# Performance work log

Measured on AMD Instinct MI355X. Metric: run time of the kernel, lower is better.

Reference implementation:

```python
import jax, jax.numpy as jnp
import numpy as np

D_MODEL = 256
B, S = 4, 4096


def setup_inputs() -> dict:
    key = jax.random.key(0)
    ks = jax.random.split(key, 6)
    k = jax.random.normal(ks[0], (B, S, D_MODEL), dtype=jnp.float32)
    q = jax.random.normal(ks[1], (B, S, D_MODEL), dtype=jnp.float32)
    v = jax.random.normal(ks[2], (B, S, D_MODEL), dtype=jnp.float32)
    # causal mask: (S, S), 1 where attending is allowed, 0 elsewhere
    mask = jnp.tril(jnp.ones((S, S), dtype=jnp.int32))
    # nn.Linear(d, d, bias=False) weights, applied as x @ W.T
    scale = 1.0 / np.sqrt(D_MODEL)
    Wk = jax.random.uniform(ks[3], (D_MODEL, D_MODEL), jnp.float32, -scale, scale)
    Wq = jax.random.uniform(ks[4], (D_MODEL, D_MODEL), jnp.float32, -scale, scale)
    Wv = jax.random.uniform(ks[5], (D_MODEL, D_MODEL), jnp.float32, -scale, scale)
    return {"k": k, "q": q, "v": v, "Wk": Wk, "Wq": Wq, "Wv": Wv, "mask": mask}


def reference(k, q, v, Wk, Wq, Wv, mask):
    # projections: nn.Linear applies x @ W.T
    key = jnp.einsum('bsd,ed->bse', k, Wk)
    query = jnp.einsum('bsd,ed->bse', q, Wq)
    value = jnp.einsum('bsd,ed->bse', v, Wv)
    # scores (b, s_q, s_k), scaled by sqrt(d_model)
    logits = jnp.einsum('bqd,bkd->bqk', query, key) / jnp.sqrt(jnp.float32(query.shape[-1]))
    logits = jnp.where(mask[None, :, :] == 0, -jnp.inf, logits)
    probs = jax.nn.softmax(logits, axis=-1)
    # dropout p=0.0 (eval) -> identity
    return jnp.einsum('bqk,bkd->bqd', probs, value)
```

## Files before the change

kernel.cpp:

```cpp
#include <hip/hip_runtime.h>


typedef __bf16 bf16_t;
typedef bf16_t bf16x8 __attribute__((ext_vector_type(8)));
typedef bf16_t bf16x4 __attribute__((ext_vector_type(4)));
typedef float  f32x4  __attribute__((ext_vector_type(4)));
typedef float  f32x16 __attribute__((ext_vector_type(16)));
typedef unsigned int u32;
typedef u32 u32x4 __attribute__((ext_vector_type(4)));

#define MFMA16(a, b, c) __builtin_amdgcn_mfma_f32_16x16x32_bf16((a), (b), (c), 0, 0, 0)
#define MFMA32(a, b, c) __builtin_amdgcn_mfma_f32_32x32x16_bf16((a), (b), (c), 0, 0, 0)

#define GLOAD_LDS16(gsrc, ldst) \
    __builtin_amdgcn_global_load_lds( \
        (const __attribute__((address_space(1))) void*)(gsrc), \
        (__attribute__((address_space(3))) void*)(ldst), 16, 0, 0)

#define NB      4
#define SEQ     4096
#define DM      256
#define NROWS   (NB * SEQ)
#define NELEM   ((size_t)NROWS * DM)
#define QSCALE  0.09016844005556021f
#define DEFER_THR 8.0f
#define SPLITG  5

__device__ __forceinline__ int swz(int row, int bytecol) {
    return bytecol ^ ((row & 7) << 4);
}

__device__ __forceinline__ u32 packbf(float a, float b) {
    union { bf16_t h; unsigned short s; } ca, cb;
    ca.h = (bf16_t)a; cb.h = (bf16_t)b;
    return (u32)ca.s | ((u32)cb.s << 16);
}

__device__ __forceinline__ bf16x8 u4_to_b8(u32x4 u) {
    union { u32x4 u; bf16x8 b; } cv; cv.u = u; return cv.b;
}

__global__ __launch_bounds__(256) void proj_kernel(
    const float* __restrict__ qin, const float* __restrict__ kin,
    const float* __restrict__ vin,
    const float* __restrict__ Wq, const float* __restrict__ Wk,
    const float* __restrict__ Wv,
    bf16_t* __restrict__ Qb, bf16_t* __restrict__ Kb, bf16_t* __restrict__ Vt)
{
    __shared__ char a_lds[128 * 64 * 2];
    __shared__ char w_lds[128 * 64 * 2];

    const int z = blockIdx.z;
    const float* in = (z == 0) ? qin : (z == 1) ? kin : vin;
    const float* W  = (z == 0) ? Wq  : (z == 1) ? Wk  : Wv;

    const int m0 = blockIdx.x * 128;
    const int n0 = blockIdx.y * 128;
    const int tid = threadIdx.x;
    const int l  = tid & 63;
    const int w  = tid >> 6;
    const int wr = w >> 1, wc = w & 1;
    const int lg = l >> 4, cl = l & 15;

    f32x4 acc[4][4] = {};

    for (int k0 = 0; k0 < DM; k0 += 64) {
#pragma unroll
        for (int i = 0; i < 8; ++i) {
            int chunk = tid + i * 256;
            int row = chunk >> 4;
            int kk  = (chunk & 15) * 4;
            float4 av = *(const float4*)(in + (size_t)(m0 + row) * DM + k0 + kk);
            bf16x4 ap;
            ap[0] = (bf16_t)av.x; ap[1] = (bf16_t)av.y;
            ap[2] = (bf16_t)av.z; ap[3] = (bf16_t)av.w;
            *(bf16x4*)(a_lds + row * 128 + swz(row, kk * 2)) = ap;

            float4 wv4 = *(const float4*)(W + (size_t)(n0 + row) * DM + k0 + kk);
            bf16x4 wp;
            wp[0] = (bf16_t)wv4.x; wp[1] = (bf16_t)wv4.y;
            wp[2] = (bf16_t)wv4.z; wp[3] = (bf16_t)wv4.w;
            *(bf16x4*)(w_lds + row * 128 + swz(row, kk * 2)) = wp;
        }
        __syncthreads();

#pragma unroll
        for (int ks = 0; ks < 2; ++ks) {
            bf16x8 af[4], bfr[4];
#pragma unroll
            for (int mi = 0; mi < 4; ++mi) {
                int row = wr * 64 + mi * 16 + cl;
                int kb2 = (ks * 32 + lg * 8) * 2;
                af[mi] = *(bf16x8*)(a_lds + row * 128 + swz(row, kb2));
            }
#pragma unroll
            for (int ni = 0; ni < 4; ++ni) {
                int row = wc * 64 + ni * 16 + cl;
                int kb2 = (ks * 32 + lg * 8) * 2;
                bfr[ni] = *(bf16x8*)(w_lds + row * 128 + swz(row, kb2));
            }
#pragma unroll
            for (int mi = 0; mi < 4; ++mi)
#pragma unroll
                for (int ni = 0; ni < 4; ++ni)
                    acc[mi][ni] = MFMA16(af[mi], bfr[ni], acc[mi][ni]);
        }
        __syncthreads();
    }

#pragma unroll
    for (int mi = 0; mi < 4; ++mi) {
#pragma unroll
        for (int ni = 0; ni < 4; ++ni) {
            int mbase = m0 + wr * 64 + mi * 16 + lg * 4;
            int ncol  = n0 + wc * 64 + ni * 16 + cl;
            if (z == 0) {
#pragma unroll
                for (int i = 0; i < 4; ++i)
                    Qb[(size_t)(mbase + i) * DM + ncol] = (bf16_t)(acc[mi][ni][i] * QSCALE);
            } else if (z == 1) {
#pragma unroll
                for (int i = 0; i < 4; ++i)
                    Kb[(size_t)(mbase + i) * DM + ncol] = (bf16_t)acc[mi][ni][i];
            } else {
                int bb = mbase >> 12;
                int s0 = mbase & 4095;
                bf16x4 pk;
                pk[0] = (bf16_t)acc[mi][ni][0]; pk[1] = (bf16_t)acc[mi][ni][1];
                pk[2] = (bf16_t)acc[mi][ni][2]; pk[3] = (bf16_t)acc[mi][ni][3];
                *(bf16x4*)(Vt + ((size_t)bb << 20) + (size_t)ncol * SEQ + s0) = pk;
            }
        }
    }
}

__global__ __launch_bounds__(128, 2) void attn_kernel(
    const bf16_t* __restrict__ Qb, const bf16_t* __restrict__ Kb,
    const bf16_t* __restrict__ Vt,
    float* __restrict__ O0, bf16_t* __restrict__ O1, float* __restrict__ ML)
{
    __shared__ __attribute__((aligned(16))) char smem[2 * 16384];

    const int g = blockIdx.x;
    const int xcd = g & 7;
    const int b = xcd >> 1;
    const int idx = ((g >> 3) << 1) | (xcd & 1);
    const int p = idx & 63;
    const int sblk = idx >> 6;

    const int tid = threadIdx.x;
    const int dhalf = tid >> 6;
    const int l = tid & 63;
    const int q5 = l & 31;
    const int hi = l >> 5;
    const int dbase = dhalf * 128;

    char* cur = smem;
    char* nxt = smem + 16384;

    const int segc[2] = { p, 127 - p };

    auto stageK = [&](int t, char* dst) {
        const size_t rbase = (size_t)(b * SEQ) + (size_t)t * 32;
#pragma unroll
        for (int i = 0; i < 8; ++i) {
            int chunk = i * 128 + tid;
            int row = chunk >> 5;
            int bc  = (chunk & 31) << 4;
            int scol = bc ^ ((row & 15) << 4);
            GLOAD_LDS16(Kb + (rbase + row) * DM + (scol >> 1), dst + chunk * 16);
        }
    };

    for (int sg = 0; sg < 2; ++sg) {
        const int c = segc[sg];
        const int qbase = c * 32;
        const int nt = c + 1;
        const int T0 = (nt * sblk) / SPLITG;
        const int T1 = (nt * (sblk + 1)) / SPLITG;
        const int qg = qbase + q5;

        __syncthreads();

        const bf16_t* qrow = Qb + (size_t)(b * SEQ + qg) * DM + hi * 8;
        bf16x8 qf[16];
#pragma unroll
        for (int ks = 0; ks < 16; ++ks)
            qf[ks] = *(const bf16x8*)(qrow + ks * 16);

        f32x16 o[4] = {};
        float m_ = -1e30f, ssum = 0.0f;

        if (T0 < T1) stageK(T0, cur);

        for (int t = T0; t < T1; ++t) {
            const int kv0 = t * 32;
            __syncthreads();

            if (t + 1 < T1) stageK(t + 1, nxt);

            const bf16_t* vbase = Vt + ((size_t)b << 20) + kv0 + hi * 8;
            bf16x8 vreg[8];
#pragma unroll
            for (int db = 0; db < 4; ++db) {
                const bf16_t* vr = vbase + (size_t)(dbase + db * 32 + q5) * SEQ;
                vreg[2 * db]     = *(const bf16x8*)(vr);
                vreg[2 * db + 1] = *(const bf16x8*)(vr + 16);
            }

            f32x16 sA = {}, sB = {};
#pragma unroll
            for (int ks = 0; ks < 16; ++ks) {
                bf16x8 kf = *(bf16x8*)(cur + q5 * 512 +
                                       ((ks * 32 + hi * 16) ^ ((q5 & 15) << 4)));
                if (ks & 1) sB = MFMA32(kf, qf[ks], sB);
                else        sA = MFMA32(kf, qf[ks], sA);
            }
            f32x16 sv = sA + sB;

            if (t == c) {
#pragma unroll
                for (int rr2 = 0; rr2 < 16; ++rr2) {
                    int kv = kv0 + (rr2 & 3) + 8 * (rr2 >> 2) + 4 * hi;
                    if (kv > qg) sv[rr2] = -1e30f;
                }
            }

            float rm = sv[0];
#pragma unroll
            for (int rr2 = 1; rr2 < 16; ++rr2) rm = fmaxf(rm, sv[rr2]);
            rm = fmaxf(rm, __shfl_xor(rm, 32));
            float mn = (rm > m_ + DEFER_THR) ? rm : m_;
            float al = exp2f(m_ - mn);
            m_ = mn;
            float rs = 0.0f;
#pragma unroll
            for (int rr2 = 0; rr2 < 16; ++rr2) { sv[rr2] = exp2f(sv[rr2] - mn); rs += sv[rr2]; }
            rs += __shfl_xor(rs, 32);
            ssum = ssum * al + rs;
            if (al != 1.0f) {
#pragma unroll
                for (int db = 0; db < 4; ++db) o[db] *= al;
            }

            u32 cpk[8], spk[8];
#pragma unroll
            for (int j = 0; j < 8; ++j) cpk[j] = packbf(sv[2 * j], sv[2 * j + 1]);
#pragma unroll
            for (int j = 0; j < 8; ++j) spk[j] = (u32)__shfl_xor((int)cpk[j], 32);
            u32x4 f0, f1;
            f0[0] = hi ? spk[2] : cpk[0];
            f0[1] = hi ? spk[3] : cpk[1];
            f0[2] = hi ? cpk[2] : spk[0];
            f0[3] = hi ? cpk[3] : spk[1];
            f1[0] = hi ? spk[6] : cpk[4];
            f1[1] = hi ? spk[7] : cpk[5];
            f1[2] = hi ? cpk[6] : spk[4];
            f1[3] = hi ? cpk[7] : spk[5];
            bf16x8 pb0 = u4_to_b8(f0);
            bf16x8 pb1 = u4_to_b8(f1);

#pragma unroll
            for (int db = 0; db < 4; ++db) {
                o[db] = MFMA32(vreg[2 * db],     pb0, o[db]);
                o[db] = MFMA32(vreg[2 * db + 1], pb1, o[db]);
            }

            char* tmp = cur; cur = nxt; nxt = tmp;
        }

        const size_t row = (size_t)(b * SEQ + qg);
        if (sblk == 0) {
#pragma unroll
            for (int db = 0; db < 4; ++db)
#pragma unroll
                for (int rr = 0; rr < 4; ++rr) {
                    int d = dbase + db * 32 + rr * 8 + hi * 4;
                    f32x4 v4 = { o[db][rr * 4 + 0], o[db][rr * 4 + 1],
                                 o[db][rr * 4 + 2], o[db][rr * 4 + 3] };
                    *(f32x4*)(O0 + row * DM + d) = v4;
                }
        } else {
            bf16_t* O1s = O1 + (size_t)(sblk - 1) * NELEM;
#pragma unroll
            for (int db = 0; db < 4; ++db)
#pragma unroll
                for (int rr = 0; rr < 4; ++rr) {
                    int d = dbase + db * 32 + rr * 8 + hi * 4;
                    bf16x4 v4;
                    v4[0] = (bf16_t)o[db][rr * 4 + 0];
                    v4[1] = (bf16_t)o[db][rr * 4 + 1];
                    v4[2] = (bf16_t)o[db][rr * 4 + 2];
                    v4[3] = (bf16_t)o[db][rr * 4 + 3];
                    *(bf16x4*)(O1s + row * DM + d) = v4;
                }
        }
        if (dhalf == 0 && hi == 0) {
            ML[(row * SPLITG + sblk) * 2 + 0] = m_;
            ML[(row * SPLITG + sblk) * 2 + 1] = ssum;
        }
    }
}

__global__ __launch_bounds__(256) void combine_kernel(
    const float* __restrict__ O0, const bf16_t* __restrict__ O1,
    const float* __restrict__ ML, float* __restrict__ out, int split)
{
    const int row = blockIdx.x * 4 + (threadIdx.x >> 6);
    const int l = threadIdx.x & 63;
    const float* mlr = ML + (size_t)row * split * 2;

    float M = -1e30f;
    for (int s = 0; s < split; ++s) M = fmaxf(M, mlr[s * 2]);
    float denom = 0.0f;
    for (int s = 0; s < split; ++s) denom += exp2f(mlr[s * 2] - M) * mlr[s * 2 + 1];
    const float inv = 1.0f / denom;

    const float w0 = exp2f(mlr[0] - M);
    f32x4 a = *(const f32x4*)(O0 + (size_t)row * DM + l * 4);
    f32x4 acc;
#pragma unroll
    for (int j = 0; j < 4; ++j) acc[j] = w0 * a[j];
    for (int s = 1; s < split; ++s) {
        float wss = exp2f(mlr[s * 2] - M);
        bf16x4 bv = *(const bf16x4*)(O1 + (size_t)(s - 1) * NELEM +
                                     (size_t)row * DM + l * 4);
#pragma unroll
        for (int j = 0; j < 4; ++j) acc[j] += wss * (float)bv[j];
    }
    f32x4 r;
#pragma unroll
    for (int j = 0; j < 4; ++j) r[j] = acc[j] * inv;
    *(f32x4*)(out + (size_t)row * DM + l * 4) = r;
}

extern "C" void kernel_launch(void* const* d_in, const int* in_sizes, int n_in,
                              void* d_out, int out_size, void* d_ws, size_t ws_size,
                              hipStream_t stream) {
    const float* k_in = (const float*)d_in[0];
    const float* q_in = (const float*)d_in[1];
    const float* v_in = (const float*)d_in[2];
    const float* Wk   = (const float*)d_in[3];
    const float* Wq   = (const float*)d_in[4];
    const float* Wv   = (const float*)d_in[5];

    bf16_t* Qb = (bf16_t*)d_ws;
    bf16_t* Kb = Qb + NELEM;
    bf16_t* Vt = Kb + NELEM;
    bf16_t* O1 = Vt + NELEM;
    float*  ML = (float*)(O1 + (size_t)(SPLITG - 1) * NELEM);
    float* outp = (float*)d_out;

    proj_kernel<<<dim3(NROWS / 128, DM / 128, 3), 256, 0, stream>>>(
        q_in, k_in, v_in, Wq, Wk, Wv, Qb, Kb, Vt);
    attn_kernel<<<4 * 64 * SPLITG, 128, 0, stream>>>(Qb, Kb, Vt, outp, O1, ML);
    combine_kernel<<<NROWS / 4, 256, 0, stream>>>(outp, O1, ML, outp, SPLITG);
}
```

Baseline: 165.2 us.

## Split attention head dim across four waves, stage Q in LDS, reduce split count

Attention blocks grow to 256 threads, with each of four waves owning 64 output columns instead of two waves owning 128. Q is staged into LDS via direct global-to-LDS loads rather than held in 16 registers, and the KV split factor drops from 5 to 3. This aims to cut register pressure and raise occupancy while reducing combine work. The trade-off is that each wave now recomputes the full QK scores, which doubles score MFMA work and adds LDS reads.

```diff
diff --git a/kernel.cpp b/kernel.cpp
--- a/kernel.cpp
+++ b/kernel.cpp
@@ -24,7 +24,7 @@
 #define NELEM   ((size_t)NROWS * DM)
 #define QSCALE  0.09016844005556021f
 #define DEFER_THR 8.0f
-#define SPLITG  5
+#define SPLITG  3
 
 __device__ __forceinline__ int swz(int row, int bytecol) {
     return bytecol ^ ((row & 7) << 4);
@@ -134,12 +134,12 @@
     }
 }
 
-__global__ __launch_bounds__(128, 2) void attn_kernel(
+__global__ __launch_bounds__(256) void attn_kernel(
     const bf16_t* __restrict__ Qb, const bf16_t* __restrict__ Kb,
     const bf16_t* __restrict__ Vt,
     float* __restrict__ O0, bf16_t* __restrict__ O1, float* __restrict__ ML)
 {
-    __shared__ __attribute__((aligned(16))) char smem[2 * 16384];
+    __shared__ __attribute__((aligned(16))) char smem[3 * 16384];
 
     const int g = blockIdx.x;
     const int xcd = g & 7;
@@ -149,22 +149,23 @@
     const int sblk = idx >> 6;
 
     const int tid = threadIdx.x;
-    const int dhalf = tid >> 6;
+    const int w = tid >> 6;
     const int l = tid & 63;
     const int q5 = l & 31;
     const int hi = l >> 5;
-    const int dbase = dhalf * 128;
-
-    char* cur = smem;
-    char* nxt = smem + 16384;
+    const int dbase = w * 64;
+
+    char* q_lds = smem;
+    char* cur = smem + 16384;
+    char* nxt = smem + 32768;
 
     const int segc[2] = { p, 127 - p };
 
     auto stageK = [&](int t, char* dst) {
         const size_t rbase = (size_t)(b * SEQ) + (size_t)t * 32;
 #pragma unroll
-        for (int i = 0; i < 8; ++i) {
-            int chunk = i * 128 + tid;
+        for (int i = 0; i < 4; ++i) {
+            int chunk = i * 256 + tid;
             int row = chunk >> 5;
             int bc  = (chunk & 31) << 4;
             int scol = bc ^ ((row & 15) << 4);
@@ -182,16 +183,21 @@
 
         __syncthreads();
 
-        const bf16_t* qrow = Qb + (size_t)(b * SEQ + qg) * DM + hi * 8;
-        bf16x8 qf[16];
-#pragma unroll
-        for (int ks = 0; ks < 16; ++ks)
-            qf[ks] = *(const bf16x8*)(qrow + ks * 16);
-
-        f32x16 o[4] = {};
+        {
+            const size_t qr0 = (size_t)(b * SEQ + qbase);
+#pragma unroll
+            for (int i = 0; i < 4; ++i) {
+                int chunk = i * 256 + tid;
+                int row = chunk >> 5;
+                int bc  = (chunk & 31) << 4;
+                int scol = bc ^ ((row & 15) << 4);
+                GLOAD_LDS16(Qb + (qr0 + row) * DM + (scol >> 1), q_lds + chunk * 16);
+            }
+        }
+        if (T0 < T1) stageK(T0, cur);
+
+        f32x16 o[2] = {};
         float m_ = -1e30f, ssum = 0.0f;
-
-        if (T0 < T1) stageK(T0, cur);
 
         for (int t = T0; t < T1; ++t) {
             const int kv0 = t * 32;
@@ -200,9 +206,9 @@
             if (t + 1 < T1) stageK(t + 1, nxt);
 
             const bf16_t* vbase = Vt + ((size_t)b << 20) + kv0 + hi * 8;
-            bf16x8 vreg[8];
-#pragma unroll
-            for (int db = 0; db < 4; ++db) {
+            bf16x8 vreg[4];
+#pragma unroll
+            for (int db = 0; db < 2; ++db) {
                 const bf16_t* vr = vbase + (size_t)(dbase + db * 32 + q5) * SEQ;
                 vreg[2 * db]     = *(const bf16x8*)(vr);
                 vreg[2 * db + 1] = *(const bf16x8*)(vr + 16);
@@ -211,10 +217,11 @@
             f32x16 sA = {}, sB = {};
 #pragma unroll
             for (int ks = 0; ks < 16; ++ks) {
-                bf16x8 kf = *(bf16x8*)(cur + q5 * 512 +
-                                       ((ks * 32 + hi * 16) ^ ((q5 & 15) << 4)));
-                if (ks & 1) sB = MFMA32(kf, qf[ks], sB);
-                else        sA = MFMA32(kf, qf[ks], sA);
+                int off = (ks * 32 + hi * 16) ^ ((q5 & 15) << 4);
+                bf16x8 kf = *(bf16x8*)(cur + q5 * 512 + off);
+                bf16x8 qv = *(bf16x8*)(q_lds + q5 * 512 + off);
+                if (ks & 1) sB = MFMA32(kf, qv, sB);
+                else        sA = MFMA32(kf, qv, sA);
             }
             f32x16 sv = sA + sB;
 
@@ -239,8 +246,8 @@
             rs += __shfl_xor(rs, 32);
             ssum = ssum * al + rs;
             if (al != 1.0f) {
-#pragma unroll
-                for (int db = 0; db < 4; ++db) o[db] *= al;
+                o[0] *= al;
+                o[1] *= al;
             }
 
             u32 cpk[8], spk[8];
@@ -261,7 +268,7 @@
             bf16x8 pb1 = u4_to_b8(f1);
 
 #pragma unroll
-            for (int db = 0; db < 4; ++db) {
+            for (int db = 0; db < 2; ++db) {
                 o[db] = MFMA32(vreg[2 * db],     pb0, o[db]);
                 o[db] = MFMA32(vreg[2 * db + 1], pb1, o[db]);
             }
@@ -272,7 +279,7 @@
         const size_t row = (size_t)(b * SEQ + qg);
         if (sblk == 0) {
 #pragma unroll
-            for (int db = 0; db < 4; ++db)
+            for (int db = 0; db < 2; ++db)
 #pragma unroll
                 for (int rr = 0; rr < 4; ++rr) {
                     int d = dbase + db * 32 + rr * 8 + hi * 4;
@@ -283,7 +290,7 @@
         } else {
             bf16_t* O1s = O1 + (size_t)(sblk - 1) * NELEM;
 #pragma unroll
-            for (int db = 0; db < 4; ++db)
+            for (int db = 0; db < 2; ++db)
 #pragma unroll
                 for (int rr = 0; rr < 4; ++rr) {
                     int d = dbase + db * 32 + rr * 8 + hi * 4;
@@ -295,7 +302,7 @@
                     *(bf16x4*)(O1s + row * DM + d) = v4;
                 }
         }
-        if (dhalf == 0 && hi == 0) {
+        if (w == 0 && hi == 0) {
             ML[(row * SPLITG + sblk) * 2 + 0] = m_;
             ML[(row * SPLITG + sblk) * 2 + 1] = ssum;
         }
@@ -353,6 +360,6 @@
 
     proj_kernel<<<dim3(NROWS / 128, DM / 128, 3), 256, 0, stream>>>(
         q_in, k_in, v_in, Wq, Wk, Wv, Qb, Kb, Vt);
-    attn_kernel<<<4 * 64 * SPLITG, 128, 0, stream>>>(Qb, Kb, Vt, outp, O1, ML);
+    attn_kernel<<<4 * 64 * SPLITG, 256, 0, stream>>>(Qb, Kb, Vt, outp, O1, ML);
     combine_kernel<<<NROWS / 4, 256, 0, stream>>>(outp, O1, ML, outp, SPLITG);
 }
```

New measurement: 185.7 us. 1.12x slower.
